# Kernel optimization log

Measured on AMD Instinct MI355X. Metric: run time of the kernel, lower is better.

## Reference

```python
import jax, jax.numpy as jnp
import numpy as np

B = 2048        # graphs per batch
NC = 81         # cells per sudoku
IN_C, HID = 10, 128
N_ACT, N_NUM, N_TECH = 4, 9, 10


def _sudoku_edges():
    idx = np.arange(NC).reshape(9, 9)
    adj = np.zeros((NC, NC), dtype=bool)
    for i in range(9):
        for j in range(9):
            n = idx[i, j]
            adj[n, idx[i, :]] = True
            adj[n, idx[:, j]] = True
            bi, bj = 3 * (i // 3), 3 * (j // 3)
            adj[n, idx[bi:bi + 3, bj:bj + 3].reshape(-1)] = True
            adj[n, n] = False
    src, dst = np.nonzero(adj)  # 1620 directed edges
    return np.stack([src, dst]).astype(np.int32)


def setup_inputs() -> dict:
    key = jax.random.key(0)
    ks = jax.random.split(key, 12)
    N = B * NC
    base = _sudoku_edges()                          # [2, 1620]
    offs = (np.arange(B, dtype=np.int32) * NC)      # [B]
    ei = (base[:, None, :] + offs[None, :, None]).reshape(2, -1)  # [2, B*1620]
    batch = np.repeat(np.arange(B, dtype=np.int32), NC)           # [N]

    def lin(k, fan_in, fan_out):
        s = 1.0 / np.sqrt(fan_in)
        return jax.random.uniform(k, (fan_in, fan_out), jnp.float32, -s, s)

    return {
        "x": jax.random.normal(ks[0], (N, IN_C), jnp.float32),
        "edge_index": jnp.asarray(ei),
        "batch": jnp.asarray(batch),
        "W1": lin(ks[1], IN_C, HID), "b1": jnp.zeros((HID,), jnp.float32),
        "W2": lin(ks[2], HID, HID),  "b2": jnp.zeros((HID,), jnp.float32),
        "Wa": lin(ks[3], HID, N_ACT),  "ba": jnp.zeros((N_ACT,), jnp.float32),
        "Wc": lin(ks[4], HID, NC),     "bc": jnp.zeros((NC,), jnp.float32),
        "Wn": lin(ks[5], HID, N_NUM),  "bn": jnp.zeros((N_NUM,), jnp.float32),
        "Wt": lin(ks[6], HID, N_TECH), "bt": jnp.zeros((N_TECH,), jnp.float32),
    }


def _gcn_conv(x, edge_index, W, b):
    n = x.shape[0]
    loop = jnp.arange(n, dtype=edge_index.dtype)
    src = jnp.concatenate([edge_index[0], loop])
    dst = jnp.concatenate([edge_index[1], loop])
    deg = jax.ops.segment_sum(jnp.ones_like(dst, jnp.float32), dst, num_segments=n)
    dinv = jax.lax.rsqrt(deg)            # deg >= 1 due to self-loops
    norm = dinv[src] * dinv[dst]         # [E+N]
    h = x @ W                            # [N, out]
    msg = h[src] * norm[:, None]         # gather + scale
    return jax.ops.segment_sum(msg, dst, num_segments=n) + b


def reference(x, edge_index, batch, W1, b1, W2, b2, Wa, ba, Wc, bc, Wn, bn, Wt, bt):
    h = jax.nn.relu(_gcn_conv(x, edge_index, W1, b1))
    h = jax.nn.relu(_gcn_conv(h, edge_index, W2, b2))
    # global mean pool over graphs
    sums = jax.ops.segment_sum(h, batch, num_segments=B)
    cnts = jax.ops.segment_sum(jnp.ones((h.shape[0],), h.dtype), batch, num_segments=B)
    pooled = sums / jnp.maximum(cnts, 1.0)[:, None]   # [B, HID]
    return (pooled @ Wa + ba, pooled @ Wc + bc, pooled @ Wn + bn, pooled @ Wt + bt)
```

## Files before the change

kernel.cpp:

```cpp
#include <hip/hip_runtime.h>
#include <hip/hip_bf16.h>

typedef __attribute__((ext_vector_type(8))) short bf16x8;
typedef __attribute__((ext_vector_type(4))) float f32x4;

__device__ __forceinline__ unsigned short f2b(float f) {
    __hip_bfloat16 h = __float2bfloat16(f);
    return __builtin_bit_cast(unsigned short, h);
}
__device__ __forceinline__ float b2f(unsigned short u) {
    unsigned v = ((unsigned)u) << 16;
    return __builtin_bit_cast(float, v);
}
__device__ __forceinline__ float ldf(const void* p, int idx, bool f32) {
    return f32 ? ((const float*)p)[idx] : b2f(((const unsigned short*)p)[idx]);
}
__device__ __forceinline__ unsigned short ldb(const void* p, int idx, bool f32) {
    return f32 ? f2b(((const float*)p)[idx]) : ((const unsigned short*)p)[idx];
}
__device__ __forceinline__ unsigned packRNE(float x, float y) {
    unsigned a = __builtin_bit_cast(unsigned, x);
    unsigned b = __builtin_bit_cast(unsigned, y);
    a += 0x7fffu + ((a >> 16) & 1u);
    b += 0x7fffu + ((b >> 16) & 1u);
    return (a >> 16) | (b & 0xffff0000u);
}

__device__ __forceinline__ bool sniff_f32(const void* x) {
    const unsigned* p = (const unsigned*)x;
    int wild = 0;
#pragma unroll
    for (int i = 0; i < 16; ++i) {
        unsigned e = (p[i] >> 7) & 0xFF;
        wild += (e != 0 && (e < 0x68 || e > 0x90)) ? 1 : 0;
    }
    return wild > 8;
}

#define WS_B1F    16
#define WS_B2F    528
#define WS_BHF    1040
#define WS_W1R    1536
#define WS_W2R    9728
#define WS_SR     42496
#define WS_WH     60928

__global__ void k_repack(const void* __restrict__ x,
                         const void* __restrict__ W1, const void* __restrict__ b1,
                         const void* __restrict__ W2, const void* __restrict__ b2,
                         const void* __restrict__ Wa, const void* __restrict__ ba,
                         const void* __restrict__ Wc, const void* __restrict__ bc,
                         const void* __restrict__ Wn, const void* __restrict__ bn,
                         const void* __restrict__ Wt, const void* __restrict__ bt,
                         char* __restrict__ ws) {
    const bool f32 = sniff_f32(x);
    const float inv21 = 1.0f / 21.0f;
    int idx = blockIdx.x * blockDim.x + threadIdx.x;
    if (idx < 4096) {
        int f = idx >> 5, k = idx & 31;
        unsigned short v = (k < 10) ? f2b(ldf(W1, k * 128 + f, f32) * inv21) : (unsigned short)0;
        ((unsigned short*)(ws + WS_W1R))[idx] = v;
        return;
    }
    idx -= 4096;
    if (idx < 16384) {
        int f = idx >> 7, k = idx & 127;
        ((unsigned short*)(ws + WS_W2R))[idx] = f2b(ldf(W2, k * 128 + f, f32) * inv21);
        return;
    }
    idx -= 16384;
    if (idx < 9216) {
        int fi = idx >> 9, rem = idx & 511;
        int lane = rem >> 3, j = rem & 7;
        int mi = fi / 3, kc = fi - mi * 3;
        int node = mi * 16 + (lane & 15);
        int cell = kc * 32 + ((lane >> 4) << 3) + j;
        bool adj = false;
        if (node < 81 && cell < 81) {
            int ni = node / 9, nj = node % 9;
            int ci = cell / 9, cj = cell % 9;
            adj = (ni == ci) || (nj == cj) ||
                  ((ni / 3 == ci / 3) && (nj / 3 == cj / 3));
        }
        ((unsigned short*)(ws + WS_SR))[idx] = adj ? (unsigned short)0x3F80 : (unsigned short)0;
        return;
    }
    idx -= 9216;
    if (idx < 13312) {
        int o = idx >> 7, f = idx & 127;
        const void* W; int oo, dim;
        if (o < 4)       { W = Wa; oo = o;      dim = 4;  }
        else if (o < 85) { W = Wc; oo = o - 4;  dim = 81; }
        else if (o < 94) { W = Wn; oo = o - 85; dim = 9;  }
        else             { W = Wt; oo = o - 94; dim = 10; }
        ((float*)(ws + WS_WH))[idx] = ldf(W, f * dim + oo, f32) * (1.0f / 81.0f);
        return;
    }
    idx -= 13312;
    if (idx < 360) {
        float v;
        if (idx < 128)      v = ldf(b1, idx, f32);
        else if (idx < 256) v = ldf(b2, idx - 128, f32);
        else {
            int o = idx - 256;
            if (o < 4)       v = ldf(ba, o, f32);
            else if (o < 85) v = ldf(bc, o - 4, f32);
            else if (o < 94) v = ldf(bn, o - 85, f32);
            else             v = ldf(bt, o - 94, f32);
        }
        if (idx < 128)      ((float*)(ws + WS_B1F))[idx] = v;
        else if (idx < 256) ((float*)(ws + WS_B2F))[idx - 128] = v;
        else                ((float*)(ws + WS_BHF))[idx - 256] = v;
    }
}

#define TS 104
#define HS 136

__global__ __launch_bounds__(128, 3) void sudoku_gnn(
    const void* __restrict__ x, const char* __restrict__ ws,
    void* __restrict__ out, int nB)
{
    __shared__ __attribute__((aligned(16))) unsigned short sG[13312];
    __shared__ float sPool[128];

    const bool f32 = sniff_f32(x);
    const unsigned short* w1r = (const unsigned short*)(ws + WS_W1R);
    const unsigned short* w2r = (const unsigned short*)(ws + WS_W2R);
    const unsigned short* sr  = (const unsigned short*)(ws + WS_SR);
    const float* b1f = (const float*)(ws + WS_B1F);
    const float* b2f = (const float*)(ws + WS_B2F);
    const float* bhf = (const float*)(ws + WS_BHF);
    const float* whf = (const float*)(ws + WS_WH);

    const int tid  = threadIdx.x;
    const int wave = tid >> 6;
    const int lane = tid & 63;
    const int ln15 = lane & 15;
    const int q    = lane >> 4;
    const int k0   = q * 8;
    const int fb   = wave * 64;
    const int g    = blockIdx.x;

    bf16x8 xf[6];
#pragma unroll
    for (int mt = 0; mt < 6; ++mt) {
        int node = mt * 16 + ln15;
        bf16x8 v = {0, 0, 0, 0, 0, 0, 0, 0};
        if (node < 81) {
            int base = (g * 81 + node) * 10;
            if (q == 0) {
#pragma unroll
                for (int jj = 0; jj < 8; ++jj) v[jj] = (short)ldb(x, base + jj, f32);
            } else if (q == 1) {
                v[0] = (short)ldb(x, base + 8, f32);
                v[1] = (short)ldb(x, base + 9, f32);
            }
        }
        xf[mt] = v;
    }
    bf16x8 w1f[4];
#pragma unroll
    for (int nt = 0; nt < 4; ++nt)
        w1f[nt] = *(const bf16x8*)&w1r[(fb + nt * 16 + ln15) * 32 + k0];

    const f32x4 z4 = {0.f, 0.f, 0.f, 0.f};
    f32x4 acc[6][4];

#pragma unroll
    for (int mt = 0; mt < 6; ++mt)
#pragma unroll
        for (int nt = 0; nt < 4; ++nt)
            acc[mt][nt] = __builtin_amdgcn_mfma_f32_16x16x32_bf16(xf[mt], w1f[nt], z4, 0, 0, 0);
#pragma unroll
    for (int mt = 0; mt < 6; ++mt)
#pragma unroll
        for (int nt = 0; nt < 4; ++nt) {
            int f = fb + nt * 16 + ln15;
            int cellb = mt * 16 + q * 4;
            *(uint2*)&sG[f * TS + cellb] =
                make_uint2(packRNE(acc[mt][nt][0], acc[mt][nt][1]),
                           packRNE(acc[mt][nt][2], acc[mt][nt][3]));
        }
    __syncthreads();

#pragma unroll
    for (int kc = 0; kc < 3; ++kc) {
        bf16x8 afr[4], sfb[6];
#pragma unroll
        for (int at = 0; at < 4; ++at)
            afr[at] = *(const bf16x8*)&sG[(fb + at * 16 + ln15) * TS + kc * 32 + k0];
#pragma unroll
        for (int jt = 0; jt < 6; ++jt)
            sfb[jt] = *(const bf16x8*)&sr[((jt * 3 + kc) * 64 + lane) * 8];
        if (kc == 0) {
#pragma unroll
            for (int jt = 0; jt < 6; ++jt)
#pragma unroll
                for (int at = 0; at < 4; ++at)
                    acc[jt][at] = __builtin_amdgcn_mfma_f32_16x16x32_bf16(afr[at], sfb[jt], z4, 0, 0, 0);
        } else {
#pragma unroll
            for (int jt = 0; jt < 6; ++jt)
#pragma unroll
                for (int at = 0; at < 4; ++at)
                    acc[jt][at] = __builtin_amdgcn_mfma_f32_16x16x32_bf16(afr[at], sfb[jt], acc[jt][at], 0, 0, 0);
        }
    }
    __syncthreads();

#pragma unroll
    for (int at = 0; at < 4; ++at) {
        float4 bv = *(const float4*)&b1f[fb + at * 16 + q * 4];
#pragma unroll
        for (int jt = 0; jt < 6; ++jt) {
            int node = jt * 16 + ln15;
            float v0 = fmaxf(acc[jt][at][0] + bv.x, 0.0f);
            float v1 = fmaxf(acc[jt][at][1] + bv.y, 0.0f);
            float v2 = fmaxf(acc[jt][at][2] + bv.z, 0.0f);
            float v3 = fmaxf(acc[jt][at][3] + bv.w, 0.0f);
            *(uint2*)&sG[node * HS + fb + at * 16 + q * 4] =
                make_uint2(packRNE(v0, v1), packRNE(v2, v3));
        }
    }
    __syncthreads();

#pragma unroll
    for (int kc = 0; kc < 4; ++kc) {
        bf16x8 a6[6], w2f[4];
#pragma unroll
        for (int mt = 0; mt < 6; ++mt)
            a6[mt] = *(const bf16x8*)&sG[(mt * 16 + ln15) * HS + kc * 32 + k0];
#pragma unroll
        for (int nt = 0; nt < 4; ++nt)
            w2f[nt] = *(const bf16x8*)&w2r[(fb + nt * 16 + ln15) * 128 + kc * 32 + k0];
        if (kc == 0) {
#pragma unroll
            for (int mt = 0; mt < 6; ++mt)
#pragma unroll
                for (int nt = 0; nt < 4; ++nt)
                    acc[mt][nt] = __builtin_amdgcn_mfma_f32_16x16x32_bf16(a6[mt], w2f[nt], z4, 0, 0, 0);
        } else {
#pragma unroll
            for (int mt = 0; mt < 6; ++mt)
#pragma unroll
                for (int nt = 0; nt < 4; ++nt)
                    acc[mt][nt] = __builtin_amdgcn_mfma_f32_16x16x32_bf16(a6[mt], w2f[nt], acc[mt][nt], 0, 0, 0);
        }
    }
    __syncthreads();

#pragma unroll
    for (int mt = 0; mt < 6; ++mt)
#pragma unroll
        for (int nt = 0; nt < 4; ++nt) {
            int f = fb + nt * 16 + ln15;
            int cellb = mt * 16 + q * 4;
            *(uint2*)&sG[f * TS + cellb] =
                make_uint2(packRNE(acc[mt][nt][0], acc[mt][nt][1]),
                           packRNE(acc[mt][nt][2], acc[mt][nt][3]));
        }
    __syncthreads();

#pragma unroll
    for (int kc = 0; kc < 3; ++kc) {
        bf16x8 afr[4], sfb[6];
#pragma unroll
        for (int at = 0; at < 4; ++at)
            afr[at] = *(const bf16x8*)&sG[(fb + at * 16 + ln15) * TS + kc * 32 + k0];
#pragma unroll
        for (int jt = 0; jt < 6; ++jt)
            sfb[jt] = *(const bf16x8*)&sr[((jt * 3 + kc) * 64 + lane) * 8];
        if (kc == 0) {
#pragma unroll
            for (int jt = 0; jt < 6; ++jt)
#pragma unroll
                for (int at = 0; at < 4; ++at)
                    acc[jt][at] = __builtin_amdgcn_mfma_f32_16x16x32_bf16(afr[at], sfb[jt], z4, 0, 0, 0);
        } else {
#pragma unroll
            for (int jt = 0; jt < 6; ++jt)
#pragma unroll
                for (int at = 0; at < 4; ++at)
                    acc[jt][at] = __builtin_amdgcn_mfma_f32_16x16x32_bf16(afr[at], sfb[jt], acc[jt][at], 0, 0, 0);
        }
    }
#pragma unroll
    for (int at = 0; at < 4; ++at) {
        float4 bv = *(const float4*)&b2f[fb + at * 16 + q * 4];
        float s0 = 0.f, s1 = 0.f, s2 = 0.f, s3 = 0.f;
#pragma unroll
        for (int jt = 0; jt < 6; ++jt) {
            int node = jt * 16 + ln15;
            if (node < 81) {
                s0 += fmaxf(acc[jt][at][0] + bv.x, 0.0f);
                s1 += fmaxf(acc[jt][at][1] + bv.y, 0.0f);
                s2 += fmaxf(acc[jt][at][2] + bv.z, 0.0f);
                s3 += fmaxf(acc[jt][at][3] + bv.w, 0.0f);
            }
        }
#pragma unroll
        for (int off = 1; off < 16; off <<= 1) {
            s0 += __shfl_xor(s0, off);
            s1 += __shfl_xor(s1, off);
            s2 += __shfl_xor(s2, off);
            s3 += __shfl_xor(s3, off);
        }
        if (ln15 == 0) {
            float4 v = {s0, s1, s2, s3};
            *(float4*)&sPool[fb + at * 16 + q * 4] = v;
        }
    }
    __syncthreads();

    if (tid < 104) {
        float a = bhf[tid];
        const float4* wrow = (const float4*)(whf + tid * 128);
        const float4* sp4  = (const float4*)sPool;
#pragma unroll 8
        for (int i = 0; i < 32; ++i) {
            float4 wv = wrow[i];
            float4 pv = sp4[i];
            a += pv.x * wv.x + pv.y * wv.y + pv.z * wv.z + pv.w * wv.w;
        }
        int o = tid, oo; size_t off;
        if (o < 4)       { oo = o;      off = (size_t)g * 4 + oo; }
        else if (o < 85) { oo = o - 4;  off = (size_t)nB * 4  + (size_t)g * 81 + oo; }
        else if (o < 94) { oo = o - 85; off = (size_t)nB * 85 + (size_t)g * 9  + oo; }
        else             { oo = o - 94; off = (size_t)nB * 94 + (size_t)g * 10 + oo; }
        if (f32) ((float*)out)[off] = a;
        else     ((unsigned short*)out)[off] = f2b(a);
    }
}

extern "C" void kernel_launch(void* const* d_in, const int* in_sizes, int n_in,
                              void* d_out, int out_size, void* d_ws, size_t ws_size,
                              hipStream_t stream) {
    const void* x  = d_in[0];
    int nB = in_sizes[2] / 81;
    if (nB <= 0) return;

    char* ws = (char*)d_ws;
    hipLaunchKernelGGL(k_repack, dim3(170), dim3(256), 0, stream,
                       x, d_in[3], d_in[4], d_in[5], d_in[6],
                       d_in[7], d_in[8], d_in[9], d_in[10],
                       d_in[11], d_in[12], d_in[13], d_in[14], ws);
    hipLaunchKernelGGL(sudoku_gnn, dim3(nB), dim3(128), 0, stream,
                       x, (const char*)ws, d_out, nB);
}
```

Measured before the change: 154.2 us.

## Split GNN block work across four waves and keep adjacency fragments in registers

Doubles the block from two to four waves. Dense transforms are split by node-tile half and feature half, and aggregation is split by 32-feature quarters, with extra barriers added before shared-buffer reuse. The adjacency operand fragments are loaded once into registers and reused across both aggregation stages. The repack kernel now stores a dtype flag, so the main kernel reads it instead of sniffing x. The aim is more waves for latency hiding and less accumulator pressure per wave, at the cost of more synchronisation and a higher register footprint from the held fragments.

Result: no change. 154.0 us (-0.1%).

```diff
diff --git a/kernel.cpp b/kernel.cpp
--- a/kernel.cpp
+++ b/kernel.cpp
@@ -25,7 +25,6 @@
     b += 0x7fffu + ((b >> 16) & 1u);
     return (a >> 16) | (b & 0xffff0000u);
 }
-
 __device__ __forceinline__ bool sniff_f32(const void* x) {
     const unsigned* p = (const unsigned*)x;
     int wild = 0;
@@ -37,6 +36,7 @@
     return wild > 8;
 }
 
+#define WS_FLAG   0
 #define WS_B1F    16
 #define WS_B2F    528
 #define WS_BHF    1040
@@ -55,6 +55,7 @@
                          char* __restrict__ ws) {
     const bool f32 = sniff_f32(x);
     const float inv21 = 1.0f / 21.0f;
+    if (blockIdx.x == 0 && threadIdx.x == 0) *(int*)(ws + WS_FLAG) = f32 ? 1 : 0;
     int idx = blockIdx.x * blockDim.x + threadIdx.x;
     if (idx < 4096) {
         int f = idx >> 5, k = idx & 31;
@@ -72,8 +73,8 @@
     if (idx < 9216) {
         int fi = idx >> 9, rem = idx & 511;
         int lane = rem >> 3, j = rem & 7;
-        int mi = fi / 3, kc = fi - mi * 3;
-        int node = mi * 16 + (lane & 15);
+        int jt = fi / 3, kc = fi - jt * 3;
+        int node = jt * 16 + (lane & 15);
         int cell = kc * 32 + ((lane >> 4) << 3) + j;
         bool adj = false;
         if (node < 81 && cell < 81) {
@@ -117,14 +118,14 @@
 #define TS 104
 #define HS 136
 
-__global__ __launch_bounds__(128, 3) void sudoku_gnn(
+__global__ __launch_bounds__(256, 2) void sudoku_gnn(
     const void* __restrict__ x, const char* __restrict__ ws,
     void* __restrict__ out, int nB)
 {
     __shared__ __attribute__((aligned(16))) unsigned short sG[13312];
     __shared__ float sPool[128];
 
-    const bool f32 = sniff_f32(x);
+    const bool f32 = (*(const int*)(ws + WS_FLAG)) != 0;
     const unsigned short* w1r = (const unsigned short*)(ws + WS_W1R);
     const unsigned short* w2r = (const unsigned short*)(ws + WS_W2R);
     const unsigned short* sr  = (const unsigned short*)(ws + WS_SR);
@@ -139,13 +140,26 @@
     const int ln15 = lane & 15;
     const int q    = lane >> 4;
     const int k0   = q * 8;
-    const int fb   = wave * 64;
+    const int mtb  = (wave & 1) * 3;
+    const int fbH  = (wave >> 1) * 64;
+    const int fQ   = wave * 32;
     const int g    = blockIdx.x;
 
-    bf16x8 xf[6];
-#pragma unroll
-    for (int mt = 0; mt < 6; ++mt) {
-        int node = mt * 16 + ln15;
+    bf16x8 sfr[3][6];
+#pragma unroll
+    for (int kc = 0; kc < 3; ++kc)
+#pragma unroll
+        for (int jt = 0; jt < 6; ++jt)
+            sfr[kc][jt] = *(const bf16x8*)&sr[((jt * 3 + kc) * 64 + lane) * 8];
+
+    bf16x8 w1f[4];
+#pragma unroll
+    for (int nt = 0; nt < 4; ++nt)
+        w1f[nt] = *(const bf16x8*)&w1r[(fbH + nt * 16 + ln15) * 32 + k0];
+    bf16x8 xf[3];
+#pragma unroll
+    for (int mt = 0; mt < 3; ++mt) {
+        int node = (mtb + mt) * 16 + ln15;
         bf16x8 v = {0, 0, 0, 0, 0, 0, 0, 0};
         if (node < 81) {
             int base = (g * 81 + node) * 10;
@@ -159,156 +173,156 @@
         }
         xf[mt] = v;
     }
-    bf16x8 w1f[4];
-#pragma unroll
-    for (int nt = 0; nt < 4; ++nt)
-        w1f[nt] = *(const bf16x8*)&w1r[(fb + nt * 16 + ln15) * 32 + k0];
 
     const f32x4 z4 = {0.f, 0.f, 0.f, 0.f};
-    f32x4 acc[6][4];
-
-#pragma unroll
-    for (int mt = 0; mt < 6; ++mt)
-#pragma unroll
-        for (int nt = 0; nt < 4; ++nt)
-            acc[mt][nt] = __builtin_amdgcn_mfma_f32_16x16x32_bf16(xf[mt], w1f[nt], z4, 0, 0, 0);
-#pragma unroll
-    for (int mt = 0; mt < 6; ++mt)
-#pragma unroll
-        for (int nt = 0; nt < 4; ++nt) {
-            int f = fb + nt * 16 + ln15;
-            int cellb = mt * 16 + q * 4;
-            *(uint2*)&sG[f * TS + cellb] =
-                make_uint2(packRNE(acc[mt][nt][0], acc[mt][nt][1]),
-                           packRNE(acc[mt][nt][2], acc[mt][nt][3]));
-        }
+
+    {
+        f32x4 accG[3][4];
+#pragma unroll
+        for (int mt = 0; mt < 3; ++mt)
+#pragma unroll
+            for (int nt = 0; nt < 4; ++nt)
+                accG[mt][nt] = __builtin_amdgcn_mfma_f32_16x16x32_bf16(xf[mt], w1f[nt], z4, 0, 0, 0);
+#pragma unroll
+        for (int mt = 0; mt < 3; ++mt)
+#pragma unroll
+            for (int nt = 0; nt < 4; ++nt) {
+                int f = fbH + nt * 16 + ln15;
+                int cellb = (mtb + mt) * 16 + q * 4;
+                *(uint2*)&sG[f * TS + cellb] =
+                    make_uint2(packRNE(accG[mt][nt][0], accG[mt][nt][1]),
+                               packRNE(accG[mt][nt][2], accG[mt][nt][3]));
+            }
+    }
     __syncthreads();
 
-#pragma unroll
-    for (int kc = 0; kc < 3; ++kc) {
-        bf16x8 afr[4], sfb[6];
-#pragma unroll
-        for (int at = 0; at < 4; ++at)
-            afr[at] = *(const bf16x8*)&sG[(fb + at * 16 + ln15) * TS + kc * 32 + k0];
-#pragma unroll
-        for (int jt = 0; jt < 6; ++jt)
-            sfb[jt] = *(const bf16x8*)&sr[((jt * 3 + kc) * 64 + lane) * 8];
-        if (kc == 0) {
-#pragma unroll
-            for (int jt = 0; jt < 6; ++jt)
-#pragma unroll
-                for (int at = 0; at < 4; ++at)
-                    acc[jt][at] = __builtin_amdgcn_mfma_f32_16x16x32_bf16(afr[at], sfb[jt], z4, 0, 0, 0);
-        } else {
-#pragma unroll
-            for (int jt = 0; jt < 6; ++jt)
-#pragma unroll
-                for (int at = 0; at < 4; ++at)
-                    acc[jt][at] = __builtin_amdgcn_mfma_f32_16x16x32_bf16(afr[at], sfb[jt], acc[jt][at], 0, 0, 0);
+    {
+        f32x4 accA[6][2];
+#pragma unroll
+        for (int kc = 0; kc < 3; ++kc) {
+            bf16x8 afr[2];
+#pragma unroll
+            for (int a2 = 0; a2 < 2; ++a2)
+                afr[a2] = *(const bf16x8*)&sG[(fQ + a2 * 16 + ln15) * TS + kc * 32 + k0];
+            if (kc == 0) {
+#pragma unroll
+                for (int jt = 0; jt < 6; ++jt)
+#pragma unroll
+                    for (int a2 = 0; a2 < 2; ++a2)
+                        accA[jt][a2] = __builtin_amdgcn_mfma_f32_16x16x32_bf16(afr[a2], sfr[0][jt], z4, 0, 0, 0);
+            } else {
+#pragma unroll
+                for (int jt = 0; jt < 6; ++jt)
+#pragma unroll
+                    for (int a2 = 0; a2 < 2; ++a2)
+                        accA[jt][a2] = __builtin_amdgcn_mfma_f32_16x16x32_bf16(afr[a2], sfr[kc][jt], accA[jt][a2], 0, 0, 0);
+            }
+        }
+        __syncthreads();
+
+#pragma unroll
+        for (int a2 = 0; a2 < 2; ++a2) {
+            float4 bv = *(const float4*)&b1f[fQ + a2 * 16 + q * 4];
+#pragma unroll
+            for (int jt = 0; jt < 6; ++jt) {
+                int node = jt * 16 + ln15;
+                float v0 = fmaxf(accA[jt][a2][0] + bv.x, 0.0f);
+                float v1 = fmaxf(accA[jt][a2][1] + bv.y, 0.0f);
+                float v2 = fmaxf(accA[jt][a2][2] + bv.z, 0.0f);
+                float v3 = fmaxf(accA[jt][a2][3] + bv.w, 0.0f);
+                *(uint2*)&sG[node * HS + fQ + a2 * 16 + q * 4] =
+                    make_uint2(packRNE(v0, v1), packRNE(v2, v3));
+            }
         }
     }
     __syncthreads();
 
-#pragma unroll
-    for (int at = 0; at < 4; ++at) {
-        float4 bv = *(const float4*)&b1f[fb + at * 16 + q * 4];
-#pragma unroll
-        for (int jt = 0; jt < 6; ++jt) {
-            int node = jt * 16 + ln15;
-            float v0 = fmaxf(acc[jt][at][0] + bv.x, 0.0f);
-            float v1 = fmaxf(acc[jt][at][1] + bv.y, 0.0f);
-            float v2 = fmaxf(acc[jt][at][2] + bv.z, 0.0f);
-            float v3 = fmaxf(acc[jt][at][3] + bv.w, 0.0f);
-            *(uint2*)&sG[node * HS + fb + at * 16 + q * 4] =
-                make_uint2(packRNE(v0, v1), packRNE(v2, v3));
-        }
+    {
+        f32x4 accG[3][4];
+#pragma unroll
+        for (int kc = 0; kc < 4; ++kc) {
+            bf16x8 w2f[4], a3[3];
+#pragma unroll
+            for (int nt = 0; nt < 4; ++nt)
+                w2f[nt] = *(const bf16x8*)&w2r[(fbH + nt * 16 + ln15) * 128 + kc * 32 + k0];
+#pragma unroll
+            for (int mt = 0; mt < 3; ++mt)
+                a3[mt] = *(const bf16x8*)&sG[((mtb + mt) * 16 + ln15) * HS + kc * 32 + k0];
+            if (kc == 0) {
+#pragma unroll
+                for (int mt = 0; mt < 3; ++mt)
+#pragma unroll
+                    for (int nt = 0; nt < 4; ++nt)
+                        accG[mt][nt] = __builtin_amdgcn_mfma_f32_16x16x32_bf16(a3[mt], w2f[nt], z4, 0, 0, 0);
+            } else {
+#pragma unroll
+                for (int mt = 0; mt < 3; ++mt)
+#pragma unroll
+                    for (int nt = 0; nt < 4; ++nt)
+                        accG[mt][nt] = __builtin_amdgcn_mfma_f32_16x16x32_bf16(a3[mt], w2f[nt], accG[mt][nt], 0, 0, 0);
+            }
+        }
+        __syncthreads();
+#pragma unroll
+        for (int mt = 0; mt < 3; ++mt)
+#pragma unroll
+            for (int nt = 0; nt < 4; ++nt) {
+                int f = fbH + nt * 16 + ln15;
+                int cellb = (mtb + mt) * 16 + q * 4;
+                *(uint2*)&sG[f * TS + cellb] =
+                    make_uint2(packRNE(accG[mt][nt][0], accG[mt][nt][1]),
+                               packRNE(accG[mt][nt][2], accG[mt][nt][3]));
+            }
     }
     __syncthreads();
 
-#pragma unroll
-    for (int kc = 0; kc < 4; ++kc) {
-        bf16x8 a6[6], w2f[4];
-#pragma unroll
-        for (int mt = 0; mt < 6; ++mt)
-            a6[mt] = *(const bf16x8*)&sG[(mt * 16 + ln15) * HS + kc * 32 + k0];
-#pragma unroll
-        for (int nt = 0; nt < 4; ++nt)
-            w2f[nt] = *(const bf16x8*)&w2r[(fb + nt * 16 + ln15) * 128 + kc * 32 + k0];
-        if (kc == 0) {
-#pragma unroll
-            for (int mt = 0; mt < 6; ++mt)
-#pragma unroll
-                for (int nt = 0; nt < 4; ++nt)
-                    acc[mt][nt] = __builtin_amdgcn_mfma_f32_16x16x32_bf16(a6[mt], w2f[nt], z4, 0, 0, 0);
-        } else {
-#pragma unroll
-            for (int mt = 0; mt < 6; ++mt)
-#pragma unroll
-                for (int nt = 0; nt < 4; ++nt)
-                    acc[mt][nt] = __builtin_amdgcn_mfma_f32_16x16x32_bf16(a6[mt], w2f[nt], acc[mt][nt], 0, 0, 0);
-        }
-    }
-    __syncthreads();
-
-#pragma unroll
-    for (int mt = 0; mt < 6; ++mt)
-#pragma unroll
-        for (int nt = 0; nt < 4; ++nt) {
-            int f = fb + nt * 16 + ln15;
-            int cellb = mt * 16 + q * 4;
-            *(uint2*)&sG[f * TS + cellb] =
-                make_uint2(packRNE(acc[mt][nt][0], acc[mt][nt][1]),
-                           packRNE(acc[mt][nt][2], acc[mt][nt][3]));
-        }
-    __syncthreads();
-
-#pragma unroll
-    for (int kc = 0; kc < 3; ++kc) {
-        bf16x8 afr[4], sfb[6];
-#pragma unroll
-        for (int at = 0; at < 4; ++at)
-            afr[at] = *(const bf16x8*)&sG[(fb + at * 16 + ln15) * TS + kc * 32 + k0];
-#pragma unroll
-        for (int jt = 0; jt < 6; ++jt)
-            sfb[jt] = *(const bf16x8*)&sr[((jt * 3 + kc) * 64 + lane) * 8];
-        if (kc == 0) {
-#pragma unroll
-            for (int jt = 0; jt < 6; ++jt)
-#pragma unroll
-                for (int at = 0; at < 4; ++at)
-                    acc[jt][at] = __builtin_amdgcn_mfma_f32_16x16x32_bf16(afr[at], sfb[jt], z4, 0, 0, 0);
-        } else {
-#pragma unroll
-            for (int jt = 0; jt < 6; ++jt)
-#pragma unroll
-                for (int at = 0; at < 4; ++at)
-                    acc[jt][at] = __builtin_amdgcn_mfma_f32_16x16x32_bf16(afr[at], sfb[jt], acc[jt][at], 0, 0, 0);
-        }
-    }
-#pragma unroll
-    for (int at = 0; at < 4; ++at) {
-        float4 bv = *(const float4*)&b2f[fb + at * 16 + q * 4];
-        float s0 = 0.f, s1 = 0.f, s2 = 0.f, s3 = 0.f;
-#pragma unroll
-        for (int jt = 0; jt < 6; ++jt) {
-            int node = jt * 16 + ln15;
-            if (node < 81) {
-                s0 += fmaxf(acc[jt][at][0] + bv.x, 0.0f);
-                s1 += fmaxf(acc[jt][at][1] + bv.y, 0.0f);
-                s2 += fmaxf(acc[jt][at][2] + bv.z, 0.0f);
-                s3 += fmaxf(acc[jt][at][3] + bv.w, 0.0f);
-            }
-        }
-#pragma unroll
-        for (int off = 1; off < 16; off <<= 1) {
-            s0 += __shfl_xor(s0, off);
-            s1 += __shfl_xor(s1, off);
-            s2 += __shfl_xor(s2, off);
-            s3 += __shfl_xor(s3, off);
-        }
-        if (ln15 == 0) {
-            float4 v = {s0, s1, s2, s3};
-            *(float4*)&sPool[fb + at * 16 + q * 4] = v;
+    {
+        f32x4 accA[6][2];
+#pragma unroll
+        for (int kc = 0; kc < 3; ++kc) {
+            bf16x8 afr[2];
+#pragma unroll
+            for (int a2 = 0; a2 < 2; ++a2)
+                afr[a2] = *(const bf16x8*)&sG[(fQ + a2 * 16 + ln15) * TS + kc * 32 + k0];
+            if (kc == 0) {
+#pragma unroll
+                for (int jt = 0; jt < 6; ++jt)
+#pragma unroll
+                    for (int a2 = 0; a2 < 2; ++a2)
+                        accA[jt][a2] = __builtin_amdgcn_mfma_f32_16x16x32_bf16(afr[a2], sfr[0][jt], z4, 0, 0, 0);
+            } else {
+#pragma unroll
+                for (int jt = 0; jt < 6; ++jt)
+#pragma unroll
+                    for (int a2 = 0; a2 < 2; ++a2)
+                        accA[jt][a2] = __builtin_amdgcn_mfma_f32_16x16x32_bf16(afr[a2], sfr[kc][jt], accA[jt][a2], 0, 0, 0);
+            }
+        }
+#pragma unroll
+        for (int a2 = 0; a2 < 2; ++a2) {
+            float4 bv = *(const float4*)&b2f[fQ + a2 * 16 + q * 4];
+            float s0 = 0.f, s1 = 0.f, s2 = 0.f, s3 = 0.f;
+#pragma unroll
+            for (int jt = 0; jt < 6; ++jt) {
+                int node = jt * 16 + ln15;
+                if (node < 81) {
+                    s0 += fmaxf(accA[jt][a2][0] + bv.x, 0.0f);
+                    s1 += fmaxf(accA[jt][a2][1] + bv.y, 0.0f);
+                    s2 += fmaxf(accA[jt][a2][2] + bv.z, 0.0f);
+                    s3 += fmaxf(accA[jt][a2][3] + bv.w, 0.0f);
+                }
+            }
+#pragma unroll
+            for (int off = 1; off < 16; off <<= 1) {
+                s0 += __shfl_xor(s0, off);
+                s1 += __shfl_xor(s1, off);
+                s2 += __shfl_xor(s2, off);
+                s3 += __shfl_xor(s3, off);
+            }
+            if (ln15 == 0) {
+                float4 v = {s0, s1, s2, s3};
+                *(float4*)&sPool[fQ + a2 * 16 + q * 4] = v;
+            }
         }
     }
     __syncthreads();
@@ -345,6 +359,6 @@
                        x, d_in[3], d_in[4], d_in[5], d_in[6],
                        d_in[7], d_in[8], d_in[9], d_in[10],
                        d_in[11], d_in[12], d_in[13], d_in[14], ws);
-    hipLaunchKernelGGL(sudoku_gnn, dim3(nB), dim3(128), 0, stream,
+    hipLaunchKernelGGL(sudoku_gnn, dim3(nB), dim3(256), 0, stream,
                        x, (const char*)ws, d_out, nB);
 }
```

## Process each graph with a single wavefront and drop all block barriers

Applied to the files above, without the earlier changes.

The fused GNN kernel now uses one 64-lane wave per graph instead of two waves, so every stage runs inside a single wave and all __syncthreads are removed. Separate shared buffers for the transposed and node-major activations replace the single reused buffer, and the adjacency fragments are loaded once and kept in registers for both aggregation passes. The f32/bf16 input sniff is done once in the repack kernel and passed through a workspace flag. In exchange, each wave does twice the MFMA work per graph, and the larger shared footprint may limit how many blocks fit per CU.

Result: slower. 173.4 us (+12.5%).

```diff
diff --git a/kernel.cpp b/kernel.cpp
--- a/kernel.cpp
+++ b/kernel.cpp
@@ -25,7 +25,6 @@
     b += 0x7fffu + ((b >> 16) & 1u);
     return (a >> 16) | (b & 0xffff0000u);
 }
-
 __device__ __forceinline__ bool sniff_f32(const void* x) {
     const unsigned* p = (const unsigned*)x;
     int wild = 0;
@@ -37,6 +36,7 @@
     return wild > 8;
 }
 
+#define WS_FLAG   0
 #define WS_B1F    16
 #define WS_B2F    528
 #define WS_BHF    1040
@@ -55,6 +55,7 @@
                          char* __restrict__ ws) {
     const bool f32 = sniff_f32(x);
     const float inv21 = 1.0f / 21.0f;
+    if (blockIdx.x == 0 && threadIdx.x == 0) *(int*)(ws + WS_FLAG) = f32 ? 1 : 0;
     int idx = blockIdx.x * blockDim.x + threadIdx.x;
     if (idx < 4096) {
         int f = idx >> 5, k = idx & 31;
@@ -72,8 +73,8 @@
     if (idx < 9216) {
         int fi = idx >> 9, rem = idx & 511;
         int lane = rem >> 3, j = rem & 7;
-        int mi = fi / 3, kc = fi - mi * 3;
-        int node = mi * 16 + (lane & 15);
+        int jt = fi / 3, kc = fi - jt * 3;
+        int node = jt * 16 + (lane & 15);
         int cell = kc * 32 + ((lane >> 4) << 3) + j;
         bool adj = false;
         if (node < 81 && cell < 81) {
@@ -117,14 +118,14 @@
 #define TS 104
 #define HS 136
 
-__global__ __launch_bounds__(128, 3) void sudoku_gnn(
+__global__ __launch_bounds__(64, 1) void sudoku_gnn(
     const void* __restrict__ x, const char* __restrict__ ws,
     void* __restrict__ out, int nB)
 {
-    __shared__ __attribute__((aligned(16))) unsigned short sG[13312];
-    __shared__ float sPool[128];
-
-    const bool f32 = sniff_f32(x);
+    __shared__ __attribute__((aligned(16))) unsigned short sT[13312];
+    __shared__ __attribute__((aligned(16))) unsigned short sH[13056];
+
+    const bool f32 = (*(const int*)(ws + WS_FLAG)) != 0;
     const unsigned short* w1r = (const unsigned short*)(ws + WS_W1R);
     const unsigned short* w2r = (const unsigned short*)(ws + WS_W2R);
     const unsigned short* sr  = (const unsigned short*)(ws + WS_SR);
@@ -133,170 +134,133 @@
     const float* bhf = (const float*)(ws + WS_BHF);
     const float* whf = (const float*)(ws + WS_WH);
 
-    const int tid  = threadIdx.x;
-    const int wave = tid >> 6;
-    const int lane = tid & 63;
+    const int lane = threadIdx.x;
     const int ln15 = lane & 15;
     const int q    = lane >> 4;
     const int k0   = q * 8;
-    const int fb   = wave * 64;
     const int g    = blockIdx.x;
-
-    bf16x8 xf[6];
-#pragma unroll
-    for (int mt = 0; mt < 6; ++mt) {
-        int node = mt * 16 + ln15;
-        bf16x8 v = {0, 0, 0, 0, 0, 0, 0, 0};
-        if (node < 81) {
-            int base = (g * 81 + node) * 10;
-            if (q == 0) {
-#pragma unroll
-                for (int jj = 0; jj < 8; ++jj) v[jj] = (short)ldb(x, base + jj, f32);
-            } else if (q == 1) {
-                v[0] = (short)ldb(x, base + 8, f32);
-                v[1] = (short)ldb(x, base + 9, f32);
+    const f32x4 z4 = {0.f, 0.f, 0.f, 0.f};
+
+    {
+        bf16x8 w1f[8];
+#pragma unroll
+        for (int nt = 0; nt < 8; ++nt)
+            w1f[nt] = *(const bf16x8*)&w1r[(nt * 16 + ln15) * 32 + k0];
+#pragma unroll
+        for (int mt = 0; mt < 6; ++mt) {
+            int node = mt * 16 + ln15;
+            bf16x8 xv = {0, 0, 0, 0, 0, 0, 0, 0};
+            if (node < 81) {
+                int base = (g * 81 + node) * 10;
+                if (q == 0) {
+#pragma unroll
+                    for (int jj = 0; jj < 8; ++jj) xv[jj] = (short)ldb(x, base + jj, f32);
+                } else if (q == 1) {
+                    xv[0] = (short)ldb(x, base + 8, f32);
+                    xv[1] = (short)ldb(x, base + 9, f32);
+                }
             }
-        }
-        xf[mt] = v;
-    }
-    bf16x8 w1f[4];
-#pragma unroll
-    for (int nt = 0; nt < 4; ++nt)
-        w1f[nt] = *(const bf16x8*)&w1r[(fb + nt * 16 + ln15) * 32 + k0];
-
-    const f32x4 z4 = {0.f, 0.f, 0.f, 0.f};
-    f32x4 acc[6][4];
-
-#pragma unroll
-    for (int mt = 0; mt < 6; ++mt)
-#pragma unroll
-        for (int nt = 0; nt < 4; ++nt)
-            acc[mt][nt] = __builtin_amdgcn_mfma_f32_16x16x32_bf16(xf[mt], w1f[nt], z4, 0, 0, 0);
-#pragma unroll
-    for (int mt = 0; mt < 6; ++mt)
-#pragma unroll
-        for (int nt = 0; nt < 4; ++nt) {
-            int f = fb + nt * 16 + ln15;
+            f32x4 a8[8];
+#pragma unroll
+            for (int nt = 0; nt < 8; ++nt)
+                a8[nt] = __builtin_amdgcn_mfma_f32_16x16x32_bf16(xv, w1f[nt], z4, 0, 0, 0);
             int cellb = mt * 16 + q * 4;
-            *(uint2*)&sG[f * TS + cellb] =
-                make_uint2(packRNE(acc[mt][nt][0], acc[mt][nt][1]),
-                           packRNE(acc[mt][nt][2], acc[mt][nt][3]));
-        }
-    __syncthreads();
-
-#pragma unroll
-    for (int kc = 0; kc < 3; ++kc) {
-        bf16x8 afr[4], sfb[6];
-#pragma unroll
-        for (int at = 0; at < 4; ++at)
-            afr[at] = *(const bf16x8*)&sG[(fb + at * 16 + ln15) * TS + kc * 32 + k0];
+#pragma unroll
+            for (int nt = 0; nt < 8; ++nt)
+                *(uint2*)&sT[(nt * 16 + ln15) * TS + cellb] =
+                    make_uint2(packRNE(a8[nt][0], a8[nt][1]), packRNE(a8[nt][2], a8[nt][3]));
+        }
+    }
+
+    bf16x8 sfr[3][6];
+#pragma unroll
+    for (int kc = 0; kc < 3; ++kc)
 #pragma unroll
         for (int jt = 0; jt < 6; ++jt)
-            sfb[jt] = *(const bf16x8*)&sr[((jt * 3 + kc) * 64 + lane) * 8];
-        if (kc == 0) {
+            sfr[kc][jt] = *(const bf16x8*)&sr[((jt * 3 + kc) * 64 + lane) * 8];
+
+#pragma unroll
+    for (int a = 0; a < 8; ++a) {
+        bf16x8 afr[3];
+#pragma unroll
+        for (int kc = 0; kc < 3; ++kc)
+            afr[kc] = *(const bf16x8*)&sT[(a * 16 + ln15) * TS + kc * 32 + k0];
+        f32x4 acc6[6];
+#pragma unroll
+        for (int jt = 0; jt < 6; ++jt)
+            acc6[jt] = __builtin_amdgcn_mfma_f32_16x16x32_bf16(afr[0], sfr[0][jt], z4, 0, 0, 0);
+#pragma unroll
+        for (int kc = 1; kc < 3; ++kc)
 #pragma unroll
             for (int jt = 0; jt < 6; ++jt)
-#pragma unroll
-                for (int at = 0; at < 4; ++at)
-                    acc[jt][at] = __builtin_amdgcn_mfma_f32_16x16x32_bf16(afr[at], sfb[jt], z4, 0, 0, 0);
-        } else {
-#pragma unroll
-            for (int jt = 0; jt < 6; ++jt)
-#pragma unroll
-                for (int at = 0; at < 4; ++at)
-                    acc[jt][at] = __builtin_amdgcn_mfma_f32_16x16x32_bf16(afr[at], sfb[jt], acc[jt][at], 0, 0, 0);
-        }
-    }
-    __syncthreads();
-
-#pragma unroll
-    for (int at = 0; at < 4; ++at) {
-        float4 bv = *(const float4*)&b1f[fb + at * 16 + q * 4];
+                acc6[jt] = __builtin_amdgcn_mfma_f32_16x16x32_bf16(afr[kc], sfr[kc][jt], acc6[jt], 0, 0, 0);
+        float4 bv = *(const float4*)&b1f[a * 16 + q * 4];
 #pragma unroll
         for (int jt = 0; jt < 6; ++jt) {
             int node = jt * 16 + ln15;
-            float v0 = fmaxf(acc[jt][at][0] + bv.x, 0.0f);
-            float v1 = fmaxf(acc[jt][at][1] + bv.y, 0.0f);
-            float v2 = fmaxf(acc[jt][at][2] + bv.z, 0.0f);
-            float v3 = fmaxf(acc[jt][at][3] + bv.w, 0.0f);
-            *(uint2*)&sG[node * HS + fb + at * 16 + q * 4] =
+            float v0 = fmaxf(acc6[jt][0] + bv.x, 0.0f);
+            float v1 = fmaxf(acc6[jt][1] + bv.y, 0.0f);
+            float v2 = fmaxf(acc6[jt][2] + bv.z, 0.0f);
+            float v3 = fmaxf(acc6[jt][3] + bv.w, 0.0f);
+            *(uint2*)&sH[node * HS + a * 16 + q * 4] =
                 make_uint2(packRNE(v0, v1), packRNE(v2, v3));
         }
     }
-    __syncthreads();
-
-#pragma unroll
-    for (int kc = 0; kc < 4; ++kc) {
-        bf16x8 a6[6], w2f[4];
-#pragma unroll
-        for (int mt = 0; mt < 6; ++mt)
-            a6[mt] = *(const bf16x8*)&sG[(mt * 16 + ln15) * HS + kc * 32 + k0];
-#pragma unroll
-        for (int nt = 0; nt < 4; ++nt)
-            w2f[nt] = *(const bf16x8*)&w2r[(fb + nt * 16 + ln15) * 128 + kc * 32 + k0];
-        if (kc == 0) {
-#pragma unroll
-            for (int mt = 0; mt < 6; ++mt)
-#pragma unroll
-                for (int nt = 0; nt < 4; ++nt)
-                    acc[mt][nt] = __builtin_amdgcn_mfma_f32_16x16x32_bf16(a6[mt], w2f[nt], z4, 0, 0, 0);
-        } else {
-#pragma unroll
-            for (int mt = 0; mt < 6; ++mt)
-#pragma unroll
-                for (int nt = 0; nt < 4; ++nt)
-                    acc[mt][nt] = __builtin_amdgcn_mfma_f32_16x16x32_bf16(a6[mt], w2f[nt], acc[mt][nt], 0, 0, 0);
-        }
-    }
-    __syncthreads();
-
-#pragma unroll
-    for (int mt = 0; mt < 6; ++mt)
-#pragma unroll
-        for (int nt = 0; nt < 4; ++nt) {
-            int f = fb + nt * 16 + ln15;
-            int cellb = mt * 16 + q * 4;
-            *(uint2*)&sG[f * TS + cellb] =
-                make_uint2(packRNE(acc[mt][nt][0], acc[mt][nt][1]),
-                           packRNE(acc[mt][nt][2], acc[mt][nt][3]));
-        }
-    __syncthreads();
-
-#pragma unroll
-    for (int kc = 0; kc < 3; ++kc) {
-        bf16x8 afr[4], sfb[6];
-#pragma unroll
-        for (int at = 0; at < 4; ++at)
-            afr[at] = *(const bf16x8*)&sG[(fb + at * 16 + ln15) * TS + kc * 32 + k0];
+
+#pragma unroll
+    for (int ntp = 0; ntp < 4; ++ntp) {
+        bf16x8 w2f[2][4];
+#pragma unroll
+        for (int t = 0; t < 2; ++t)
+#pragma unroll
+            for (int kc = 0; kc < 4; ++kc)
+                w2f[t][kc] = *(const bf16x8*)&w2r[((ntp * 2 + t) * 16 + ln15) * 128 + kc * 32 + k0];
+#pragma unroll
+        for (int mt = 0; mt < 6; ++mt) {
+            bf16x8 a3[4];
+#pragma unroll
+            for (int kc = 0; kc < 4; ++kc)
+                a3[kc] = *(const bf16x8*)&sH[(mt * 16 + ln15) * HS + kc * 32 + k0];
+#pragma unroll
+            for (int t = 0; t < 2; ++t) {
+                f32x4 acc = __builtin_amdgcn_mfma_f32_16x16x32_bf16(a3[0], w2f[t][0], z4, 0, 0, 0);
+#pragma unroll
+                for (int kc = 1; kc < 4; ++kc)
+                    acc = __builtin_amdgcn_mfma_f32_16x16x32_bf16(a3[kc], w2f[t][kc], acc, 0, 0, 0);
+                int f = (ntp * 2 + t) * 16 + ln15;
+                int cellb = mt * 16 + q * 4;
+                *(uint2*)&sT[f * TS + cellb] =
+                    make_uint2(packRNE(acc[0], acc[1]), packRNE(acc[2], acc[3]));
+            }
+        }
+    }
+
+    float* pool = (float*)sH;
+#pragma unroll
+    for (int a = 0; a < 8; ++a) {
+        bf16x8 afr[3];
+#pragma unroll
+        for (int kc = 0; kc < 3; ++kc)
+            afr[kc] = *(const bf16x8*)&sT[(a * 16 + ln15) * TS + kc * 32 + k0];
+        f32x4 acc6[6];
 #pragma unroll
         for (int jt = 0; jt < 6; ++jt)
-            sfb[jt] = *(const bf16x8*)&sr[((jt * 3 + kc) * 64 + lane) * 8];
-        if (kc == 0) {
+            acc6[jt] = __builtin_amdgcn_mfma_f32_16x16x32_bf16(afr[0], sfr[0][jt], z4, 0, 0, 0);
+#pragma unroll
+        for (int kc = 1; kc < 3; ++kc)
 #pragma unroll
             for (int jt = 0; jt < 6; ++jt)
-#pragma unroll
-                for (int at = 0; at < 4; ++at)
-                    acc[jt][at] = __builtin_amdgcn_mfma_f32_16x16x32_bf16(afr[at], sfb[jt], z4, 0, 0, 0);
-        } else {
-#pragma unroll
-            for (int jt = 0; jt < 6; ++jt)
-#pragma unroll
-                for (int at = 0; at < 4; ++at)
-                    acc[jt][at] = __builtin_amdgcn_mfma_f32_16x16x32_bf16(afr[at], sfb[jt], acc[jt][at], 0, 0, 0);
-        }
-    }
-#pragma unroll
-    for (int at = 0; at < 4; ++at) {
-        float4 bv = *(const float4*)&b2f[fb + at * 16 + q * 4];
+                acc6[jt] = __builtin_amdgcn_mfma_f32_16x16x32_bf16(afr[kc], sfr[kc][jt], acc6[jt], 0, 0, 0);
+        float4 bv = *(const float4*)&b2f[a * 16 + q * 4];
         float s0 = 0.f, s1 = 0.f, s2 = 0.f, s3 = 0.f;
 #pragma unroll
         for (int jt = 0; jt < 6; ++jt) {
             int node = jt * 16 + ln15;
             if (node < 81) {
-                s0 += fmaxf(acc[jt][at][0] + bv.x, 0.0f);
-                s1 += fmaxf(acc[jt][at][1] + bv.y, 0.0f);
-                s2 += fmaxf(acc[jt][at][2] + bv.z, 0.0f);
-                s3 += fmaxf(acc[jt][at][3] + bv.w, 0.0f);
+                s0 += fmaxf(acc6[jt][0] + bv.x, 0.0f);
+                s1 += fmaxf(acc6[jt][1] + bv.y, 0.0f);
+                s2 += fmaxf(acc6[jt][2] + bv.z, 0.0f);
+                s3 += fmaxf(acc6[jt][3] + bv.w, 0.0f);
             }
         }
 #pragma unroll
@@ -308,28 +272,31 @@
         }
         if (ln15 == 0) {
             float4 v = {s0, s1, s2, s3};
-            *(float4*)&sPool[fb + at * 16 + q * 4] = v;
-        }
-    }
-    __syncthreads();
-
-    if (tid < 104) {
-        float a = bhf[tid];
-        const float4* wrow = (const float4*)(whf + tid * 128);
-        const float4* sp4  = (const float4*)sPool;
+            *(float4*)&pool[a * 16 + q * 4] = v;
+        }
+    }
+
+    const float4* sp4 = (const float4*)pool;
+#pragma unroll
+    for (int pass = 0; pass < 2; ++pass) {
+        int o = lane + pass * 64;
+        if (o < 104) {
+            float a = bhf[o];
+            const float4* wrow = (const float4*)(whf + o * 128);
 #pragma unroll 8
-        for (int i = 0; i < 32; ++i) {
-            float4 wv = wrow[i];
-            float4 pv = sp4[i];
-            a += pv.x * wv.x + pv.y * wv.y + pv.z * wv.z + pv.w * wv.w;
-        }
-        int o = tid, oo; size_t off;
-        if (o < 4)       { oo = o;      off = (size_t)g * 4 + oo; }
-        else if (o < 85) { oo = o - 4;  off = (size_t)nB * 4  + (size_t)g * 81 + oo; }
-        else if (o < 94) { oo = o - 85; off = (size_t)nB * 85 + (size_t)g * 9  + oo; }
-        else             { oo = o - 94; off = (size_t)nB * 94 + (size_t)g * 10 + oo; }
-        if (f32) ((float*)out)[off] = a;
-        else     ((unsigned short*)out)[off] = f2b(a);
+            for (int i = 0; i < 32; ++i) {
+                float4 wv = wrow[i];
+                float4 pv = sp4[i];
+                a += pv.x * wv.x + pv.y * wv.y + pv.z * wv.z + pv.w * wv.w;
+            }
+            int oo; size_t off;
+            if (o < 4)       { oo = o;      off = (size_t)g * 4 + oo; }
+            else if (o < 85) { oo = o - 4;  off = (size_t)nB * 4  + (size_t)g * 81 + oo; }
+            else if (o < 94) { oo = o - 85; off = (size_t)nB * 85 + (size_t)g * 9  + oo; }
+            else             { oo = o - 94; off = (size_t)nB * 94 + (size_t)g * 10 + oo; }
+            if (f32) ((float*)out)[off] = a;
+            else     ((unsigned short*)out)[off] = f2b(a);
+        }
     }
 }
 
@@ -345,6 +312,6 @@
                        x, d_in[3], d_in[4], d_in[5], d_in[6],
                        d_in[7], d_in[8], d_in[9], d_in[10],
                        d_in[11], d_in[12], d_in[13], d_in[14], ws);
-    hipLaunchKernelGGL(sudoku_gnn, dim3(nB), dim3(128), 0, stream,
+    hipLaunchKernelGGL(sudoku_gnn, dim3(nB), dim3(64), 0, stream,
                        x, (const char*)ws, d_out, nB);
 }
```
